# Kernel tuning notes

Measured on AMD Instinct MI355X. Metric: run time of the kernel, lower is better.

Reference implementation:

```python
import jax, jax.numpy as jnp
import numpy as np


def conv1x1(x, w, b):
    # x: (B, C_in, D, H, W), w: (C_out, C_in), b: (C_out,)  -- 1x1x1 Conv3d == per-voxel linear
    return jnp.einsum('bcdhw,oc->bodhw', x, w) + b[None, :, None, None, None]


def setup_inputs() -> dict:
    key = jax.random.key(0)
    ks = jax.random.split(key, 6)
    B, C, D, H, W = 2, 64, 8, 64, 64
    K = 4096  # codebook_size after halving
    return {
        'z': jax.random.normal(ks[0], (B, C, D, H, W), dtype=jnp.float32),
        'embedding': jax.random.normal(ks[1], (K, C), dtype=jnp.float32),
        'pre_w': jax.random.normal(ks[2], (C, C), dtype=jnp.float32) * (1.0 / np.sqrt(C)),
        'pre_b': jax.random.normal(ks[3], (C,), dtype=jnp.float32) * 0.01,
        'post_w': jax.random.normal(ks[4], (C, C), dtype=jnp.float32) * (1.0 / np.sqrt(C)),
        'post_b': jax.random.normal(ks[5], (C,), dtype=jnp.float32) * 0.01,
    }


def reference(z, embedding, pre_w, pre_b, post_w, post_b):
    B, C, D, H, W = z.shape
    x = conv1x1(z, pre_w, pre_b)  # pre_quant_conv

    # ---- quantize() ----
    # tokens: (B*D*H*W, C)
    t = jnp.transpose(x, (0, 2, 3, 4, 1)).reshape(-1, C)
    # squared euclidean distances (argmin identical to torch.cdist argmin)
    dist2 = (jnp.sum(t * t, axis=-1, keepdims=True)
             - 2.0 * t @ embedding.T
             + jnp.sum(embedding * embedding, axis=-1)[None, :])  # (N, K)
    idx = jnp.argmin(dist2, axis=-1)  # (N,)
    q = embedding[idx]  # gather: (N, C)

    commitment_loss = jnp.mean((jax.lax.stop_gradient(q) - t) ** 2)
    codebook_loss = jnp.mean((q - jax.lax.stop_gradient(t)) ** 2)

    # straight-through estimator
    q = t + jax.lax.stop_gradient(q - t)
    quant = jnp.transpose(q.reshape(B, D, H, W, C), (0, 4, 1, 2, 3))

    out = conv1x1(quant, post_w, post_b)  # post_quant_conv
    indices = idx.reshape(B, D, H, W)
    return out, codebook_loss, commitment_loss, indices
```

## Files before the change

### kernel.cpp

```cpp
#include <hip/hip_runtime.h>
#include <cstdint>
#include <cstddef>

typedef float  f32x4  __attribute__((ext_vector_type(4)));
typedef float  f32x16 __attribute__((ext_vector_type(16)));
typedef short  s16x8  __attribute__((ext_vector_type(8)));

#define DEV __device__ __forceinline__

static constexpr int    DHW       = 32768;
static constexpr int    NTOK      = 65536;
static constexpr int    CHUNK_B   = 18432;
static constexpr size_t OUT_ELEMS = 4194304;
static constexpr float  BIGC      = 512.0f;
static constexpr float  TAU       = 0.015f;
static constexpr int    FLAG_CAP  = 7424;

static constexpr size_t WS_PREP = 0;
static constexpr size_t WS_RESW = 1179648;
static constexpr size_t WS_RESB = 2228224;
static constexpr size_t WS_PART = 2490368;
static constexpr size_t WS_CNT  = 2494464;
static constexpr size_t WS_FLAG = 2494720;

DEV unsigned f2bf(float f) {
  unsigned u = __float_as_uint(f);
  return (u + 0x7FFFu + ((u >> 16) & 1u)) >> 16;
}
DEV float bf2f(unsigned h) { return __uint_as_float(h << 16); }
DEV unsigned med3u(unsigned a, unsigned b, unsigned c) {
  unsigned r;
  asm("v_med3_u32 %0, %1, %2, %3" : "=v"(r) : "v"(a), "v"(b), "v"(c));
  return r;
}
DEV void gl_lds16(const void* g, void* l) {
  __builtin_amdgcn_global_load_lds(
      (const __attribute__((address_space(1))) unsigned int*)g,
      (__attribute__((address_space(3))) unsigned int*)l, 16, 0, 0);
}

__global__ __launch_bounds__(256) void k_pre(const float* __restrict__ z,
    const float* __restrict__ emb, const float* __restrict__ pw, const float* __restrict__ pb,
    float* __restrict__ dout, char* __restrict__ ws)
{
  const int blk = blockIdx.x, tid = threadIdx.x;
  if (blk == 0 && tid == 0) *(int*)(ws + WS_CNT) = 0;
  if (blk < 512) {
    float* t = dout;
    const int v = (blk & 255) * 256 + tid;
    const int half = blk >> 8;
    const int b = v >> 15, r = v & (DHW - 1);
    const float* zp = z + (size_t)b * 64 * DHW + r;
    float zr[64];
#pragma unroll
    for (int c2 = 0; c2 < 64; ++c2) zr[c2] = zp[(size_t)c2 * DHW];
    const int c0 = half * 32;
    for (int c = c0; c < c0 + 32; c += 4) {
      const float* w0 = pw + c * 64;
      const float* w1 = pw + (c + 1) * 64;
      const float* w2 = pw + (c + 2) * 64;
      const float* w3 = pw + (c + 3) * 64;
      float a0 = pb[c], a1 = pb[c + 1], a2 = pb[c + 2], a3 = pb[c + 3];
#pragma unroll
      for (int c2 = 0; c2 < 64; ++c2) {
        const float zv = zr[c2];
        a0 = fmaf(w0[c2], zv, a0); a1 = fmaf(w1[c2], zv, a1);
        a2 = fmaf(w2[c2], zv, a2); a3 = fmaf(w3[c2], zv, a3);
      }
      t[(size_t)c * NTOK + v]       = a0;
      t[(size_t)(c + 1) * NTOK + v] = a1;
      t[(size_t)(c + 2) * NTOK + v] = a2;
      t[(size_t)(c + 3) * NTOK + v] = a3;
    }
  } else {
    const int tt = (blk - 512) * 256 + tid;
#pragma unroll
    for (int uu = 0; uu < 2; ++uu) {
      const int u = tt * 2 + uu;
      const int k = u >> 3, j = u & 7;
      const float* ep = emb + (size_t)k * 64 + j * 8;
      unsigned hw[4], lw[4];
#pragma unroll
      for (int i = 0; i < 4; ++i) {
        float g0 = -2.0f * ep[2 * i], g1 = -2.0f * ep[2 * i + 1];
        unsigned h0 = f2bf(g0); unsigned l0 = f2bf(g0 - bf2f(h0));
        unsigned h1 = f2bf(g1); unsigned l1 = f2bf(g1 - bf2f(h1));
        hw[i] = h0 | (h1 << 16); lw[i] = l0 | (l1 << 16);
      }
      char* base = ws + WS_PREP + (size_t)(k >> 6) * CHUNK_B;
      const int r = k & 63;
      const int swz = (r & 15) << 4;
      char* rowp = base + r * 256;
      *(uint4*)(rowp + ((j * 16) ^ swz))        = make_uint4(hw[0], hw[1], hw[2], hw[3]);
      *(uint4*)(rowp + ((128 + j * 16) ^ swz))  = make_uint4(lw[0], lw[1], lw[2], lw[3]);
      if (j == 0) {
        const float* er = emb + (size_t)k * 64;
        float s = 0.f;
#pragma unroll
        for (int c = 0; c < 64; ++c) s = fmaf(er[c], er[c], s);
        s += BIGC;
        unsigned eh  = f2bf(s);
        float    rs  = s - bf2f(eh);
        unsigned el  = f2bf(rs);
        unsigned el2 = f2bf(rs - bf2f(el));
        *(uint4*)(base + 16384 + r * 16) = make_uint4(eh | (el << 16), el2, 0u, 0u);
        if (r == 0) *(uint4*)(base + 16384 + 1024) = make_uint4(0u, 0u, 0u, 0u);
      }
    }
  }
}

__global__ __launch_bounds__(1024, 4) void k_dist(float* __restrict__ dout,
                                                  char* __restrict__ ws)
{
  constexpr int NCH = 16;
  __shared__ __align__(16) char smem[2 * CHUNK_B];
  const float* t = dout;
  const int tid = threadIdx.x;
  const int w = tid >> 6, lane = tid & 63;
  const int l31 = lane & 31, khalf = lane >> 5;
  const int gidx = blockIdx.x >> 2, h = blockIdx.x & 3;
  const int tb = gidx * 512 + w * 32;
  const int tok = tb + l31;

  s16x8 tav[4], tlv[4];
#pragma unroll
  for (int kt = 0; kt < 4; ++kt) {
    const float* tc = t + (size_t)(kt * 16 + khalf * 8) * NTOK + tok;
    float f[8];
#pragma unroll
    for (int i = 0; i < 8; ++i) f[i] = tc[(size_t)i * NTOK];
    union { unsigned u[4]; s16x8 v; } xh, xl;
#pragma unroll
    for (int i = 0; i < 4; ++i) {
      unsigned h0 = f2bf(f[2 * i]),     l0 = f2bf(f[2 * i]     - bf2f(h0));
      unsigned h1 = f2bf(f[2 * i + 1]), l1 = f2bf(f[2 * i + 1] - bf2f(h1));
      xh.u[i] = h0 | (h1 << 16); xl.u[i] = l0 | (l1 << 16);
    }
    tav[kt] = xh.v; tlv[kt] = xl.v;
  }
  s16x8 ones;
  { union { unsigned u[4]; s16x8 v; } o;
    o.u[0] = khalf ? 0u : 0x3F803F80u;
    o.u[1] = khalf ? 0u : 0x00003F80u;
    o.u[2] = 0u; o.u[3] = 0u; ones = o.v; }

  const char* prep = ws + WS_PREP + (size_t)h * NCH * CHUNK_B;
  const int swz = (l31 & 15) << 4;

  auto stage = [&](int cc) {
    const char* src = prep + (size_t)cc * CHUNK_B;
    char* dst = smem + (size_t)(cc & 1) * CHUNK_B;
    gl_lds16(src + w * 1024 + lane * 16, dst + w * 1024);
    if (w < 2) gl_lds16(src + 16384 + w * 1024 + lane * 16, dst + 16384 + w * 1024);
  };
  stage(0);
  __syncthreads();

  unsigned u1 = 0x7f800000u, u2 = 0x7f800000u;
  int c1 = 0;

  for (int c = 0; c < NCH; ++c) {
    const char* L = smem + (c & 1) * CHUNK_B;
    if (c + 1 < NCH) stage(c + 1);
    f32x16 acc0 = {}, acc1 = {};
    {
      const s16x8 e0 = *(const s16x8*)(L + (khalf ? (16384 + 1024) : (16384 + l31 * 16)));
      const s16x8 e1 = *(const s16x8*)(L + (khalf ? (16384 + 1024) : (16384 + (32 + l31) * 16)));
      acc0 = __builtin_amdgcn_mfma_f32_32x32x16_bf16(e0, ones, acc0, 0, 0, 0);
      acc1 = __builtin_amdgcn_mfma_f32_32x32x16_bf16(e1, ones, acc1, 0, 0, 0);
    }
#pragma unroll
    for (int kt = 0; kt < 4; ++kt) {
      const int i0 = (kt * 32 + khalf * 16) ^ swz;
      const s16x8 gh0 = *(const s16x8*)(L + l31 * 256 + i0);
      const s16x8 gl0 = *(const s16x8*)(L + l31 * 256 + (i0 ^ 128));
      const s16x8 gh1 = *(const s16x8*)(L + (32 + l31) * 256 + i0);
      const s16x8 gl1 = *(const s16x8*)(L + (32 + l31) * 256 + (i0 ^ 128));
      acc0 = __builtin_amdgcn_mfma_f32_32x32x16_bf16(gh0, tav[kt], acc0, 0, 0, 0);
      acc0 = __builtin_amdgcn_mfma_f32_32x32x16_bf16(gh0, tlv[kt], acc0, 0, 0, 0);
      acc0 = __builtin_amdgcn_mfma_f32_32x32x16_bf16(gl0, tav[kt], acc0, 0, 0, 0);
      acc1 = __builtin_amdgcn_mfma_f32_32x32x16_bf16(gh1, tav[kt], acc1, 0, 0, 0);
      acc1 = __builtin_amdgcn_mfma_f32_32x32x16_bf16(gh1, tlv[kt], acc1, 0, 0, 0);
      acc1 = __builtin_amdgcn_mfma_f32_32x32x16_bf16(gl1, tav[kt], acc1, 0, 0, 0);
    }
    const unsigned p1 = u1;
#pragma unroll
    for (int q = 0; q < 16; ++q) {
      const unsigned w0 = (unsigned)((q & 3) + 8 * (q >> 2));
      unsigned v0 = (__float_as_uint(acc0[q]) & ~63u) | w0;
      u2 = med3u(u1, v0, u2); u1 = u1 < v0 ? u1 : v0;
      unsigned v1 = (__float_as_uint(acc1[q]) & ~63u) | (w0 + 32u);
      u2 = med3u(u1, v1, u2); u1 = u1 < v1 ? u1 : v1;
    }
    if (u1 != p1) c1 = c;
    __syncthreads();
  }

  u1 |= (unsigned)(khalf * 4);
  const unsigned o1 = __shfl_xor(u1, 32);
  const unsigned o2 = __shfl_xor(u2, 32);
  const int      oc = __shfl_xor(c1, 32);
  const unsigned am = u1 & ~63u, om = o1 & ~63u;
  const int mycode = c1 * 64 + (int)(u1 & 63u);
  const int ocode  = oc * 64 + (int)(o1 & 63u);
  const bool owins = (om < am) || (om == am && ocode < mycode);
  const unsigned f1 = owins ? o1 : u1;
  const int      fc = owins ? oc : c1;
  const unsigned mx = owins ? am : om;
  unsigned s2 = (u2 & ~63u) < (o2 & ~63u) ? (u2 & ~63u) : (o2 & ~63u);
  s2 = s2 < mx ? s2 : mx;
  if (khalf == 0) {
    const bool nt = (__uint_as_float(s2) - __uint_as_float(f1 & ~63u)) < TAU;
    ((unsigned*)(ws + WS_RESW))[h * 65536 + tok] = f1;
    ((unsigned char*)(ws + WS_RESB))[h * 65536 + tok] =
        (unsigned char)(fc | (nt ? 0x80 : 0));
  }
}

__global__ __launch_bounds__(256) void k_merge(const float* __restrict__ emb,
    float* __restrict__ dout, char* __restrict__ ws)
{
  __shared__ float ls[4];
  const int tid = threadIdx.x;
  const int v = blockIdx.x * 64 + (tid >> 2);
  const int q4 = tid & 3;
  const unsigned* resw = (const unsigned*)(ws + WS_RESW);
  const unsigned char* resb = (const unsigned char*)(ws + WS_RESB);
  unsigned k1 = 0xffffffffu, k2 = 0xffffffffu, bw = 0; int bq = 0;
#pragma unroll
  for (int q = 0; q < 4; ++q) {
    const unsigned W = resw[q * 65536 + v];
    const unsigned key = W & ~63u;
    if (key < k1) { k2 = k1; k1 = key; bq = q; bw = W; }
    else          { k2 = key < k2 ? key : k2; }
  }
  const unsigned char bb = resb[bq * 65536 + v];
  const int code = bq * 1024 + (int)(bb & 15u) * 64 + (int)(bw & 63u);
  const float* tcol = dout + v;
  const float* qe = emb + (size_t)code * 64 + q4 * 16;
  float acc = 0.f;
#pragma unroll
  for (int i = 0; i < 4; ++i) {
    const float4 qv = *(const float4*)(qe + i * 4);
#pragma unroll
    for (int j = 0; j < 4; ++j) {
      const int ch = q4 * 16 + i * 4 + j;
      const float d = tcol[(size_t)ch * NTOK] - ((const float*)&qv)[j];
      acc = fmaf(d, d, acc);
    }
  }
  acc += __shfl_xor(acc, 1);
  acc += __shfl_xor(acc, 2);
  if (q4 == 0) {
    dout[OUT_ELEMS + 2 + v] = (float)code;
    const bool flag = (bb & 0x80u) ||
                      (__uint_as_float(k2) - __uint_as_float(k1) < TAU);
    if (flag) {
      int p = atomicAdd((int*)(ws + WS_CNT), 1);
      if (p < FLAG_CAP) ((int*)(ws + WS_FLAG))[p] = v;
    }
  }
#pragma unroll
  for (int m = 4; m < 64; m <<= 1) acc += __shfl_xor(acc, m);
  const int lane = tid & 63, wv = tid >> 6;
  if (lane == 0) ls[wv] = acc;
  __syncthreads();
  if (tid == 0)
    ((float*)(ws + WS_PART))[blockIdx.x] = ls[0] + ls[1] + ls[2] + ls[3];
}

__global__ __launch_bounds__(256) void k_refine(const float* __restrict__ z,
    const float* __restrict__ emb, const float* __restrict__ pw, const float* __restrict__ pb,
    float* __restrict__ dout, char* __restrict__ ws)
{
  __shared__ double tdsh[64];
  __shared__ double dred[4]; __shared__ int kred[4];
  int cv = *(const int*)(ws + WS_CNT);
  if (cv > FLAG_CAP) cv = FLAG_CAP;
  const int tid = threadIdx.x;
  const int lane = tid & 63, wv = tid >> 6;

  for (int slot = blockIdx.x; slot < cv; slot += 256) {
    const int n = ((const int*)(ws + WS_FLAG))[slot];

    if (tid < 64) {
      const int b = n >> 15, r = n & (DHW - 1);
      const float* zp = z + (size_t)b * 64 * DHW + r;
      const float* wr = pw + tid * 64;
      double a = (double)pb[tid];
      for (int c2 = 0; c2 < 64; ++c2)
        a = fma((double)wr[c2], (double)zp[(size_t)c2 * DHW], a);
      tdsh[tid] = a;
    }
    __syncthreads();

    double td[64];
#pragma unroll
    for (int j = 0; j < 64; ++j) td[j] = tdsh[j];

    double dmin = 1e300; int kmin = 0;
    for (int it = 0; it < 16; ++it) {
      const int code = it * 256 + tid;
      const float4* e = (const float4*)(emb + (size_t)code * 64);
      double d0 = 0.0, d1 = 0.0;
#pragma unroll
      for (int i = 0; i < 16; ++i) {
        const float4 ev = e[i];
        const double x0 = td[4 * i]     - (double)ev.x; d0 = fma(x0, x0, d0);
        const double x1 = td[4 * i + 1] - (double)ev.y; d1 = fma(x1, x1, d1);
        const double x2 = td[4 * i + 2] - (double)ev.z; d0 = fma(x2, x2, d0);
        const double x3 = td[4 * i + 3] - (double)ev.w; d1 = fma(x3, x3, d1);
      }
      const double d = d0 + d1;
      if (d < dmin) { dmin = d; kmin = code; }
    }
#pragma unroll
    for (int m = 1; m < 64; m <<= 1) {
      const double od = __shfl_xor(dmin, m);
      const int    ok = __shfl_xor(kmin, m);
      if (od < dmin || (od == dmin && ok < kmin)) { dmin = od; kmin = ok; }
    }
    if (lane == 0) { dred[wv] = dmin; kred[wv] = kmin; }
    __syncthreads();
    if (tid == 0) {
#pragma unroll
      for (int i = 1; i < 4; ++i)
        if (dred[i] < dmin || (dred[i] == dmin && kred[i] < kmin)) { dmin = dred[i]; kmin = kred[i]; }
      dout[OUT_ELEMS + 2 + n] = (float)kmin;
    }
    __syncthreads();
  }
}

__global__ __launch_bounds__(256) void k_post(const float* __restrict__ emb,
    const float* __restrict__ ow, const float* __restrict__ ob,
    float* __restrict__ dout, const char* __restrict__ ws)
{
  __shared__ float ps[256];
  const int v = (blockIdx.x & 255) * 256 + threadIdx.x;
  const int half = blockIdx.x >> 8;
  const int b = v >> 15, r = v & (DHW - 1);
  const int code = (int)dout[OUT_ELEMS + 2 + v];
  const float* q = emb + (size_t)code * 64;
  float qr[64];
#pragma unroll
  for (int i = 0; i < 16; ++i) *(float4*)(qr + i * 4) = *(const float4*)(q + i * 4);
  float* op = dout + (size_t)b * 64 * DHW + r;
  const int o0 = half * 32;
  for (int o = o0; o < o0 + 32; o += 4) {
    const float* w0 = ow + o * 64;
    const float* w1 = ow + (o + 1) * 64;
    const float* w2 = ow + (o + 2) * 64;
    const float* w3 = ow + (o + 3) * 64;
    float a0 = ob[o], a1 = ob[o + 1], a2 = ob[o + 2], a3 = ob[o + 3];
#pragma unroll
    for (int cch = 0; cch < 64; ++cch) {
      const float qv = qr[cch];
      a0 = fmaf(w0[cch], qv, a0); a1 = fmaf(w1[cch], qv, a1);
      a2 = fmaf(w2[cch], qv, a2); a3 = fmaf(w3[cch], qv, a3);
    }
    op[(size_t)o * DHW]       = a0;
    op[(size_t)(o + 1) * DHW] = a1;
    op[(size_t)(o + 2) * DHW] = a2;
    op[(size_t)(o + 3) * DHW] = a3;
  }
  if (blockIdx.x == 0) {
    const float* part = (const float*)(ws + WS_PART);
    const int t4 = threadIdx.x * 4;
    float s = ((part[t4] + part[t4 + 1]) + part[t4 + 2]) + part[t4 + 3];
    ps[threadIdx.x] = s;
    __syncthreads();
    if (threadIdx.x == 0) {
      float tot = 0.f;
      for (int i = 0; i < 256; ++i) tot += ps[i];
      const float mean = tot / 4194304.0f;
      dout[OUT_ELEMS]     = mean;
      dout[OUT_ELEMS + 1] = mean;
    }
  }
}

extern "C" void kernel_launch(void* const* d_in, const int* in_sizes, int n_in,
                              void* d_out, int out_size, void* d_ws, size_t ws_size,
                              hipStream_t stream) {
  (void)in_sizes; (void)n_in; (void)out_size; (void)ws_size;
  const float* z   = (const float*)d_in[0];
  const float* emb = (const float*)d_in[1];
  const float* pw  = (const float*)d_in[2];
  const float* pb  = (const float*)d_in[3];
  const float* ow  = (const float*)d_in[4];
  const float* ob  = (const float*)d_in[5];
  float* out = (float*)d_out;
  char*  ws  = (char*)d_ws;

  hipLaunchKernelGGL(k_pre,    dim3(576),  dim3(256),  0, stream, z, emb, pw, pb, out, ws);
  hipLaunchKernelGGL(k_dist,   dim3(512),  dim3(1024), 0, stream, out, ws);
  hipLaunchKernelGGL(k_merge,  dim3(1024), dim3(256),  0, stream, emb, out, ws);
  hipLaunchKernelGGL(k_refine, dim3(256),  dim3(256),  0, stream, z, emb, pw, pb, out, ws);
  hipLaunchKernelGGL(k_post,   dim3(512),  dim3(256),  0, stream, emb, ow, ob, out, ws);
}
```

Measured before the change: 179.4 us.

## Stage codebook chunks in groups of four and split argmin tracking chains

Result: no change. 181.2 us (+1.0%).

```diff
diff --git a/kernel.cpp b/kernel.cpp
--- a/kernel.cpp
+++ b/kernel.cpp
@@ -113,8 +113,7 @@
 __global__ __launch_bounds__(1024, 4) void k_dist(float* __restrict__ dout,
                                                   char* __restrict__ ws)
 {
-  constexpr int NCH = 16;
-  __shared__ __align__(16) char smem[2 * CHUNK_B];
+  __shared__ __align__(16) char smem[2 * 65536];
   const float* t = dout;
   const int tid = threadIdx.x;
   const int w = tid >> 6, lane = tid & 63;
@@ -145,59 +144,81 @@
     o.u[1] = khalf ? 0u : 0x00003F80u;
     o.u[2] = 0u; o.u[3] = 0u; ones = o.v; }
 
-  const char* prep = ws + WS_PREP + (size_t)h * NCH * CHUNK_B;
+  const char* prep = ws + WS_PREP + (size_t)h * 16 * CHUNK_B;
   const int swz = (l31 & 15) << 4;
 
-  auto stage = [&](int cc) {
-    const char* src = prep + (size_t)cc * CHUNK_B;
-    char* dst = smem + (size_t)(cc & 1) * CHUNK_B;
-    gl_lds16(src + w * 1024 + lane * 16, dst + w * 1024);
-    if (w < 2) gl_lds16(src + 16384 + w * 1024 + lane * 16, dst + 16384 + w * 1024);
+  auto stageg = [&](int g) {
+#pragma unroll
+    for (int k = 0; k < 4; ++k) {
+      const int cc = g * 4 + k;
+      gl_lds16(prep + (size_t)cc * CHUNK_B + w * 1024 + lane * 16,
+               smem + (size_t)(g & 1) * 65536 + k * 16384 + w * 1024);
+    }
   };
-  stage(0);
+
+  unsigned u1a = 0x7f800000u, u2a = 0x7f800000u;
+  unsigned u1b = 0x7f800000u, u2b = 0x7f800000u;
+  int c1a = 0, c1b = 0;
+
+  stageg(0);
   __syncthreads();
-
-  unsigned u1 = 0x7f800000u, u2 = 0x7f800000u;
-  int c1 = 0;
-
-  for (int c = 0; c < NCH; ++c) {
-    const char* L = smem + (c & 1) * CHUNK_B;
-    if (c + 1 < NCH) stage(c + 1);
-    f32x16 acc0 = {}, acc1 = {};
-    {
-      const s16x8 e0 = *(const s16x8*)(L + (khalf ? (16384 + 1024) : (16384 + l31 * 16)));
-      const s16x8 e1 = *(const s16x8*)(L + (khalf ? (16384 + 1024) : (16384 + (32 + l31) * 16)));
-      acc0 = __builtin_amdgcn_mfma_f32_32x32x16_bf16(e0, ones, acc0, 0, 0, 0);
-      acc1 = __builtin_amdgcn_mfma_f32_32x32x16_bf16(e1, ones, acc1, 0, 0, 0);
-    }
-#pragma unroll
-    for (int kt = 0; kt < 4; ++kt) {
-      const int i0 = (kt * 32 + khalf * 16) ^ swz;
-      const s16x8 gh0 = *(const s16x8*)(L + l31 * 256 + i0);
-      const s16x8 gl0 = *(const s16x8*)(L + l31 * 256 + (i0 ^ 128));
-      const s16x8 gh1 = *(const s16x8*)(L + (32 + l31) * 256 + i0);
-      const s16x8 gl1 = *(const s16x8*)(L + (32 + l31) * 256 + (i0 ^ 128));
-      acc0 = __builtin_amdgcn_mfma_f32_32x32x16_bf16(gh0, tav[kt], acc0, 0, 0, 0);
-      acc0 = __builtin_amdgcn_mfma_f32_32x32x16_bf16(gh0, tlv[kt], acc0, 0, 0, 0);
-      acc0 = __builtin_amdgcn_mfma_f32_32x32x16_bf16(gl0, tav[kt], acc0, 0, 0, 0);
-      acc1 = __builtin_amdgcn_mfma_f32_32x32x16_bf16(gh1, tav[kt], acc1, 0, 0, 0);
-      acc1 = __builtin_amdgcn_mfma_f32_32x32x16_bf16(gh1, tlv[kt], acc1, 0, 0, 0);
-      acc1 = __builtin_amdgcn_mfma_f32_32x32x16_bf16(gl1, tav[kt], acc1, 0, 0, 0);
-    }
-    const unsigned p1 = u1;
-#pragma unroll
-    for (int q = 0; q < 16; ++q) {
-      const unsigned w0 = (unsigned)((q & 3) + 8 * (q >> 2));
-      unsigned v0 = (__float_as_uint(acc0[q]) & ~63u) | w0;
-      u2 = med3u(u1, v0, u2); u1 = u1 < v0 ? u1 : v0;
-      unsigned v1 = (__float_as_uint(acc1[q]) & ~63u) | (w0 + 32u);
-      u2 = med3u(u1, v1, u2); u1 = u1 < v1 ? u1 : v1;
-    }
-    if (u1 != p1) c1 = c;
+  for (int g = 0; g < 4; ++g) {
+    if (g + 1 < 4) stageg(g + 1);
+#pragma unroll
+    for (int k = 0; k < 4; ++k) {
+      const int c = g * 4 + k;
+      const char* L = smem + (size_t)(g & 1) * 65536 + k * 16384;
+      const char* e2p = prep + (size_t)c * CHUNK_B + 16384;
+      f32x16 acc0 = {}, acc1 = {};
+      {
+        const s16x8 e0 = *(const s16x8*)(e2p + (khalf ? 1024 : l31 * 16));
+        const s16x8 e1 = *(const s16x8*)(e2p + (khalf ? 1024 : (32 + l31) * 16));
+        acc0 = __builtin_amdgcn_mfma_f32_32x32x16_bf16(e0, ones, acc0, 0, 0, 0);
+        acc1 = __builtin_amdgcn_mfma_f32_32x32x16_bf16(e1, ones, acc1, 0, 0, 0);
+      }
+#pragma unroll
+      for (int kt = 0; kt < 4; ++kt) {
+        const int i0 = (kt * 32 + khalf * 16) ^ swz;
+        const s16x8 gh0 = *(const s16x8*)(L + l31 * 256 + i0);
+        const s16x8 gl0 = *(const s16x8*)(L + l31 * 256 + (i0 ^ 128));
+        const s16x8 gh1 = *(const s16x8*)(L + (32 + l31) * 256 + i0);
+        const s16x8 gl1 = *(const s16x8*)(L + (32 + l31) * 256 + (i0 ^ 128));
+        acc0 = __builtin_amdgcn_mfma_f32_32x32x16_bf16(gh0, tav[kt], acc0, 0, 0, 0);
+        acc0 = __builtin_amdgcn_mfma_f32_32x32x16_bf16(gh0, tlv[kt], acc0, 0, 0, 0);
+        acc0 = __builtin_amdgcn_mfma_f32_32x32x16_bf16(gl0, tav[kt], acc0, 0, 0, 0);
+        acc1 = __builtin_amdgcn_mfma_f32_32x32x16_bf16(gh1, tav[kt], acc1, 0, 0, 0);
+        acc1 = __builtin_amdgcn_mfma_f32_32x32x16_bf16(gh1, tlv[kt], acc1, 0, 0, 0);
+        acc1 = __builtin_amdgcn_mfma_f32_32x32x16_bf16(gl1, tav[kt], acc1, 0, 0, 0);
+      }
+      const unsigned pa = u1a, pb = u1b;
+#pragma unroll
+      for (int q = 0; q < 16; ++q) {
+        const unsigned w0 = (unsigned)((q & 3) + 8 * (q >> 2));
+        unsigned v0 = (__float_as_uint(acc0[q]) & ~63u) | w0;
+        u2a = med3u(u1a, v0, u2a); u1a = u1a < v0 ? u1a : v0;
+        unsigned v1 = (__float_as_uint(acc1[q]) & ~63u) | (w0 + 32u);
+        u2b = med3u(u1b, v1, u2b); u1b = u1b < v1 ? u1b : v1;
+      }
+      if (u1a != pa) c1a = c;
+      if (u1b != pb) c1b = c;
+    }
     __syncthreads();
   }
 
-  u1 |= (unsigned)(khalf * 4);
+  u1a |= (unsigned)(khalf * 4);
+  u1b |= (unsigned)(khalf * 4);
+  unsigned u1, u2; int c1;
+  {
+    const unsigned am = u1a & ~63u, bm = u1b & ~63u;
+    const int codeA = c1a * 64 + (int)(u1a & 63u);
+    const int codeB = c1b * 64 + (int)(u1b & 63u);
+    const bool bwins = (bm < am) || (bm == am && codeB < codeA);
+    u1 = bwins ? u1b : u1a;
+    c1 = bwins ? c1b : c1a;
+    const unsigned mx = bwins ? am : bm;
+    unsigned s = (u2a & ~63u) < (u2b & ~63u) ? (u2a & ~63u) : (u2b & ~63u);
+    u2 = s < mx ? s : mx;
+  }
   const unsigned o1 = __shfl_xor(u1, 32);
   const unsigned o2 = __shfl_xor(u2, 32);
   const int      oc = __shfl_xor(c1, 32);
```

## Derive quantization loss from argmin distance and split pre/post convs into quarters

Applied to the files above, without the earlier changes.

Result: faster. 171.5 us (median of 2 runs) (-4.4%).

```diff
diff --git a/kernel.cpp b/kernel.cpp
--- a/kernel.cpp
+++ b/kernel.cpp
@@ -45,17 +45,17 @@
 {
   const int blk = blockIdx.x, tid = threadIdx.x;
   if (blk == 0 && tid == 0) *(int*)(ws + WS_CNT) = 0;
-  if (blk < 512) {
+  if (blk < 1024) {
     float* t = dout;
     const int v = (blk & 255) * 256 + tid;
-    const int half = blk >> 8;
+    const int qtr = blk >> 8;
     const int b = v >> 15, r = v & (DHW - 1);
     const float* zp = z + (size_t)b * 64 * DHW + r;
     float zr[64];
 #pragma unroll
     for (int c2 = 0; c2 < 64; ++c2) zr[c2] = zp[(size_t)c2 * DHW];
-    const int c0 = half * 32;
-    for (int c = c0; c < c0 + 32; c += 4) {
+    const int c0 = qtr * 16;
+    for (int c = c0; c < c0 + 16; c += 4) {
       const float* w0 = pw + c * 64;
       const float* w1 = pw + (c + 1) * 64;
       const float* w2 = pw + (c + 2) * 64;
@@ -73,7 +73,7 @@
       t[(size_t)(c + 3) * NTOK + v] = a3;
     }
   } else {
-    const int tt = (blk - 512) * 256 + tid;
+    const int tt = (blk - 1024) * 256 + tid;
 #pragma unroll
     for (int uu = 0; uu < 2; ++uu) {
       const int u = tt * 2 + uu;
@@ -115,6 +115,7 @@
 {
   constexpr int NCH = 16;
   __shared__ __align__(16) char smem[2 * CHUNK_B];
+  __shared__ float t2s[16];
   const float* t = dout;
   const int tid = threadIdx.x;
   const int w = tid >> 6, lane = tid & 63;
@@ -124,12 +125,15 @@
   const int tok = tb + l31;
 
   s16x8 tav[4], tlv[4];
+  float t2 = 0.f;
 #pragma unroll
   for (int kt = 0; kt < 4; ++kt) {
     const float* tc = t + (size_t)(kt * 16 + khalf * 8) * NTOK + tok;
     float f[8];
 #pragma unroll
     for (int i = 0; i < 8; ++i) f[i] = tc[(size_t)i * NTOK];
+#pragma unroll
+    for (int i = 0; i < 8; ++i) t2 = fmaf(f[i], f[i], t2);
     union { unsigned u[4]; s16x8 v; } xh, xl;
 #pragma unroll
     for (int i = 0; i < 4; ++i) {
@@ -139,6 +143,11 @@
     }
     tav[kt] = xh.v; tlv[kt] = xl.v;
   }
+  t2 += __shfl_xor(t2, 32);
+#pragma unroll
+  for (int m = 1; m <= 16; m <<= 1) t2 += __shfl_xor(t2, m);
+  if (lane == 0) t2s[w] = t2;
+
   s16x8 ones;
   { union { unsigned u[4]; s16x8 v; } o;
     o.u[0] = khalf ? 0u : 0x3F803F80u;
@@ -216,15 +225,20 @@
     ((unsigned char*)(ws + WS_RESB))[h * 65536 + tok] =
         (unsigned char)(fc | (nt ? 0x80 : 0));
   }
-}
-
-__global__ __launch_bounds__(256) void k_merge(const float* __restrict__ emb,
-    float* __restrict__ dout, char* __restrict__ ws)
+  if (h == 0 && tid == 0) {
+    float s = 0.f;
+#pragma unroll
+    for (int i = 0; i < 16; ++i) s += t2s[i];
+    ((float*)(ws + WS_PART))[256 + gidx] = s;
+  }
+}
+
+__global__ __launch_bounds__(256) void k_merge(float* __restrict__ dout,
+                                               char* __restrict__ ws)
 {
   __shared__ float ls[4];
   const int tid = threadIdx.x;
-  const int v = blockIdx.x * 64 + (tid >> 2);
-  const int q4 = tid & 3;
+  const int v = blockIdx.x * 256 + tid;
   const unsigned* resw = (const unsigned*)(ws + WS_RESW);
   const unsigned char* resb = (const unsigned char*)(ws + WS_RESB);
   unsigned k1 = 0xffffffffu, k2 = 0xffffffffu, bw = 0; int bq = 0;
@@ -237,32 +251,16 @@
   }
   const unsigned char bb = resb[bq * 65536 + v];
   const int code = bq * 1024 + (int)(bb & 15u) * 64 + (int)(bw & 63u);
-  const float* tcol = dout + v;
-  const float* qe = emb + (size_t)code * 64 + q4 * 16;
-  float acc = 0.f;
-#pragma unroll
-  for (int i = 0; i < 4; ++i) {
-    const float4 qv = *(const float4*)(qe + i * 4);
-#pragma unroll
-    for (int j = 0; j < 4; ++j) {
-      const int ch = q4 * 16 + i * 4 + j;
-      const float d = tcol[(size_t)ch * NTOK] - ((const float*)&qv)[j];
-      acc = fmaf(d, d, acc);
-    }
-  }
-  acc += __shfl_xor(acc, 1);
-  acc += __shfl_xor(acc, 2);
-  if (q4 == 0) {
-    dout[OUT_ELEMS + 2 + v] = (float)code;
-    const bool flag = (bb & 0x80u) ||
-                      (__uint_as_float(k2) - __uint_as_float(k1) < TAU);
-    if (flag) {
-      int p = atomicAdd((int*)(ws + WS_CNT), 1);
-      if (p < FLAG_CAP) ((int*)(ws + WS_FLAG))[p] = v;
-    }
-  }
-#pragma unroll
-  for (int m = 4; m < 64; m <<= 1) acc += __shfl_xor(acc, m);
+  dout[OUT_ELEMS + 2 + v] = (float)code;
+  const bool flag = (bb & 0x80u) ||
+                    (__uint_as_float(k2) - __uint_as_float(k1) < TAU);
+  if (flag) {
+    int p = atomicAdd((int*)(ws + WS_CNT), 1);
+    if (p < FLAG_CAP) ((int*)(ws + WS_FLAG))[p] = v;
+  }
+  float acc = __uint_as_float(k1) - 512.0f;
+#pragma unroll
+  for (int m = 1; m <= 32; m <<= 1) acc += __shfl_xor(acc, m);
   const int lane = tid & 63, wv = tid >> 6;
   if (lane == 0) ls[wv] = acc;
   __syncthreads();
@@ -339,7 +337,7 @@
 {
   __shared__ float ps[256];
   const int v = (blockIdx.x & 255) * 256 + threadIdx.x;
-  const int half = blockIdx.x >> 8;
+  const int qtr = blockIdx.x >> 8;
   const int b = v >> 15, r = v & (DHW - 1);
   const int code = (int)dout[OUT_ELEMS + 2 + v];
   const float* q = emb + (size_t)code * 64;
@@ -347,8 +345,8 @@
 #pragma unroll
   for (int i = 0; i < 16; ++i) *(float4*)(qr + i * 4) = *(const float4*)(q + i * 4);
   float* op = dout + (size_t)b * 64 * DHW + r;
-  const int o0 = half * 32;
-  for (int o = o0; o < o0 + 32; o += 4) {
+  const int o0 = qtr * 16;
+  for (int o = o0; o < o0 + 16; o += 4) {
     const float* w0 = ow + o * 64;
     const float* w1 = ow + (o + 1) * 64;
     const float* w2 = ow + (o + 2) * 64;
@@ -368,7 +366,9 @@
   if (blockIdx.x == 0) {
     const float* part = (const float*)(ws + WS_PART);
     const int t4 = threadIdx.x * 4;
-    float s = ((part[t4] + part[t4 + 1]) + part[t4 + 2]) + part[t4 + 3];
+    float s = 0.f;
+    if (threadIdx.x < 96)
+      s = ((part[t4] + part[t4 + 1]) + part[t4 + 2]) + part[t4 + 3];
     ps[threadIdx.x] = s;
     __syncthreads();
     if (threadIdx.x == 0) {
@@ -394,9 +394,9 @@
   float* out = (float*)d_out;
   char*  ws  = (char*)d_ws;
 
-  hipLaunchKernelGGL(k_pre,    dim3(576),  dim3(256),  0, stream, z, emb, pw, pb, out, ws);
+  hipLaunchKernelGGL(k_pre,    dim3(1088), dim3(256),  0, stream, z, emb, pw, pb, out, ws);
   hipLaunchKernelGGL(k_dist,   dim3(512),  dim3(1024), 0, stream, out, ws);
-  hipLaunchKernelGGL(k_merge,  dim3(1024), dim3(256),  0, stream, emb, out, ws);
+  hipLaunchKernelGGL(k_merge,  dim3(256),  dim3(256),  0, stream, out, ws);
   hipLaunchKernelGGL(k_refine, dim3(256),  dim3(256),  0, stream, z, emb, pw, pb, out, ws);
-  hipLaunchKernelGGL(k_post,   dim3(512),  dim3(256),  0, stream, emb, ow, ob, out, ws);
-}
+  hipLaunchKernelGGL(k_post,   dim3(1024), dim3(256),  0, stream, emb, ow, ob, out, ws);
+}
```
